# Kernel tuning notes

Measured on AMD Instinct MI355X. Metric: run time of the kernel, lower is better.

The kernel has to match this reference:

```python
import jax, jax.numpy as jnp
import numpy as np

N = 100000   # nodes
E = 1600000  # edges
IN = 128     # input feature dim
HID = 64     # hidden = IN // 2
OUT = 8      # output_size
B = 16384    # lookup batch


def sage_conv(x, src, dst, W_l, W_r, b, n):
    # PyG SAGEConv (aggr='mean', root_weight=True):
    # out = lin_l(mean_{j in N(i)} x_j) + lin_r(x_i)
    msgs = x[src]                                              # [E, F] gather
    agg = jax.ops.segment_sum(msgs, dst, num_segments=n)       # [N, F] scatter-add
    deg = jax.ops.segment_sum(jnp.ones((src.shape[0],), x.dtype), dst, num_segments=n)
    mean = agg / jnp.maximum(deg, 1.0)[:, None]                # zero-degree -> 0
    return mean @ W_l + x @ W_r + b


def setup_inputs() -> dict:
    key = jax.random.key(0)
    ks = jax.random.split(key, 10)
    node_feats = jax.random.normal(ks[0], (N, IN), dtype=jnp.float32)
    edge_index = jax.random.randint(ks[1], (2, E), 0, N, dtype=jnp.int64)
    idx = jax.random.randint(ks[2], (B,), 0, N, dtype=jnp.int64)
    dropout_mask = jax.random.uniform(ks[3], (N, HID), dtype=jnp.float32)
    s1 = 1.0 / np.sqrt(IN)
    s2 = 1.0 / np.sqrt(HID)
    W1_l = jax.random.normal(ks[4], (IN, HID), dtype=jnp.float32) * s1
    W1_r = jax.random.normal(ks[5], (IN, HID), dtype=jnp.float32) * s1
    b1 = jnp.zeros((HID,), dtype=jnp.float32)
    W2_l = jax.random.normal(ks[6], (HID, OUT), dtype=jnp.float32) * s2
    W2_r = jax.random.normal(ks[7], (HID, OUT), dtype=jnp.float32) * s2
    b2 = jnp.zeros((OUT,), dtype=jnp.float32)
    return {"node_feats": node_feats, "edge_index": edge_index, "idx": idx,
            "dropout_mask": dropout_mask, "W1_l": W1_l, "W1_r": W1_r, "b1": b1,
            "W2_l": W2_l, "W2_r": W2_r, "b2": b2}


def reference(node_feats, edge_index, idx, dropout_mask, W1_l, W1_r, b1, W2_l, W2_r, b2):
    n = node_feats.shape[0]
    src, dst = edge_index[0], edge_index[1]
    h = sage_conv(node_feats, src, dst, W1_l, W1_r, b1, n)     # [N, HID]
    h = jax.nn.relu(h)
    keep = (dropout_mask > 0.5).astype(h.dtype)                # F.dropout p=0.5
    h = h * keep * 2.0                                         # inverted dropout scale 1/(1-p)
    emb = sage_conv(h, src, dst, W2_l, W2_r, b2, n)            # [N, OUT]
    return emb[idx]                                            # [B, OUT]
```

## Files before the change

### kernel.cpp

```cpp
#include <hip/hip_runtime.h>
#include <hip/hip_fp16.h>

#define IN_F 128
#define HID_F 64
#define OUT_F 8

#define BSHIFT 7
#define BGRAN 128
#define BCAP 2688
#define NBUK_MAX 784
#define CHUNK 4096
#define EPT (CHUNK / 256)
#define CEPT ((BCAP + 255) / 256)

typedef _Float16 f16x8 __attribute__((ext_vector_type(8)));
typedef float f32x4 __attribute__((ext_vector_type(4)));

__global__ __launch_bounds__(1024) void init_bcur(int* __restrict__ bcur, int nbuk) {
  int t = threadIdx.x;
  if (t < nbuk) bcur[t] = t * BCAP;
}

__global__ __launch_bounds__(256) void bucket_scatter(
    const int* __restrict__ src, const int* __restrict__ dst,
    int* __restrict__ bcur, int* __restrict__ ebuf, int n_edges) {
  __shared__ int hist[NBUK_MAX];
  __shared__ int base[NBUK_MAX];
  int t = threadIdx.x;
  for (int i = t; i < NBUK_MAX; i += 256) hist[i] = 0;
  __syncthreads();
  int e0 = blockIdx.x * CHUNK;
  int pk[EPT];
  int bk[EPT];
#pragma unroll
  for (int k = 0; k < EPT; ++k) {
    int e = e0 + k * 256 + t;
    if (e < n_edges) {
      int s = src[e];
      int d = dst[e];
      bk[k] = d >> BSHIFT;
      pk[k] = ((d & (BGRAN - 1)) << 24) | s;
      atomicAdd(&hist[bk[k]], 1);
    } else {
      bk[k] = -1;
    }
  }
  __syncthreads();
  for (int i = t; i < NBUK_MAX; i += 256) {
    int c = hist[i];
    base[i] = c ? atomicAdd(&bcur[i], c) : 0;
  }
  __syncthreads();
  for (int i = t; i < NBUK_MAX; i += 256) hist[i] = 0;
  __syncthreads();
#pragma unroll
  for (int k = 0; k < EPT; ++k) {
    if (bk[k] >= 0) {
      int r = atomicAdd(&hist[bk[k]], 1);
      ebuf[base[bk[k]] + r] = pk[k];
    }
  }
}

__global__ __launch_bounds__(256) void bucket_csr(
    const int* __restrict__ ebuf, const int* __restrict__ bcur,
    int* __restrict__ offs_f, int* __restrict__ deg_i,
    int* __restrict__ csr_src, int n_nodes) {
  __shared__ int hist[BGRAN];
  __shared__ int cur[BGRAN];
  __shared__ int s[BGRAN];
  __shared__ int lds_src[BCAP];
  int b = blockIdx.x;
  int t = threadIdx.x;
  if (t < BGRAN) hist[t] = 0;
  __syncthreads();
  int beg = b * BCAP;
  int cnt = bcur[b] - beg;
  int pk[CEPT];
  int np = 0;
  for (int j = t; j < cnt; j += 256) {
    pk[np] = ebuf[beg + j];
    atomicAdd(&hist[(unsigned)pk[np] >> 24], 1);
    ++np;
  }
  __syncthreads();
  if (t < BGRAN) s[t] = hist[t];
  __syncthreads();
  for (int d = 1; d < BGRAN; d <<= 1) {
    int v = 0;
    if (t >= d && t < BGRAN) v = s[t - d];
    __syncthreads();
    if (t >= d && t < BGRAN) s[t] += v;
    __syncthreads();
  }
  if (t < BGRAN) {
    int excl = (t == 0) ? 0 : s[t - 1];
    cur[t] = excl;
    int node = b * BGRAN + t;
    if (node < n_nodes) {
      offs_f[node] = beg + excl;
      deg_i[node] = hist[t];
    }
  }
  __syncthreads();
  for (int i = 0; i < np; ++i) {
    int dl = (unsigned)pk[i] >> 24;
    int p = atomicAdd(&cur[dl], 1);
    lds_src[p] = pk[i] & 0xFFFFFF;
  }
  __syncthreads();
  for (int j = t; j < cnt; j += 256) csr_src[beg + j] = lds_src[j];
}

__global__ __launch_bounds__(128) void w_prep(
    const float* __restrict__ Wl, const float* __restrict__ Wr,
    _Float16* __restrict__ Wt) {
  int n = threadIdx.x;
  for (int k = 0; k < IN_F; ++k) {
    float v = (n < HID_F) ? Wl[k * HID_F + n] : Wr[k * HID_F + (n - HID_F)];
    Wt[n * IN_F + k] = (_Float16)v;
  }
}

#define K1_ROWS 128
#define XSH 136
__global__ __launch_bounds__(256) void k1_proj(
    const float* __restrict__ x,
    const _Float16* __restrict__ Wt,
    const float* __restrict__ b1,
    const float* __restrict__ mask,
    __half* __restrict__ y1h,
    __half* __restrict__ r1h,
    unsigned long long* __restrict__ mbits,
    int n_nodes) {
  __shared__ _Float16 XS[K1_ROWS * XSH];
  int tid = threadIdx.x;
  int w = tid >> 6;
  int lane = tid & 63;
  int n0 = blockIdx.x * K1_ROWS;
  int m = lane & 15;
  int quad = lane >> 4;

  for (int i = w * 32; i < w * 32 + 32; ++i) {
    int node = n0 + i;
    if (node < n_nodes) {
      float mv = mask[(size_t)node * HID_F + lane];
      unsigned long long bits = __ballot(mv > 0.5f);
      if (lane == 0) mbits[node] = bits;
    }
  }

  f16x8 af[2][4];
#pragma unroll
  for (int ti = 0; ti < 2; ++ti) {
    int t = w + ti * 4;
#pragma unroll
    for (int kk = 0; kk < 4; ++kk)
      af[ti][kk] = *(const f16x8*)(Wt + (size_t)(t * 16 + m) * IN_F + kk * 32 + quad * 8);
  }
  float4 b1v = *(const float4*)(b1 + w * 16 + quad * 4);

#pragma unroll
  for (int p = 0; p < 16; ++p) {
    int i = tid + p * 256;
    int row = i >> 5;
    int k4 = (i & 31) * 4;
    int gs = min(n0 + row, n_nodes - 1);
    float4 v = *(const float4*)(x + (size_t)gs * IN_F + k4);
    _Float16 hv[4] = {(_Float16)v.x, (_Float16)v.y, (_Float16)v.z, (_Float16)v.w};
    *(uint2*)&XS[row * XSH + k4] = *(uint2*)hv;
  }
  __syncthreads();

#pragma unroll
  for (int rt = 0; rt < 8; ++rt) {
    f32x4 acc0 = f32x4{0.f, 0.f, 0.f, 0.f};
    f32x4 acc1 = f32x4{0.f, 0.f, 0.f, 0.f};
#pragma unroll
    for (int kk = 0; kk < 4; ++kk) {
      f16x8 bx = *(const f16x8*)&XS[(rt * 16 + m) * XSH + kk * 32 + quad * 8];
      acc0 = __builtin_amdgcn_mfma_f32_16x16x32_f16(af[0][kk], bx, acc0, 0, 0, 0);
      acc1 = __builtin_amdgcn_mfma_f32_16x16x32_f16(af[1][kk], bx, acc1, 0, 0, 0);
    }
    int node = n0 + rt * 16 + m;
    if (node < n_nodes) {
      __half hy[4], hr[4];
#pragma unroll
      for (int r = 0; r < 4; ++r) {
        hy[r] = __float2half(acc0[r]);
        hr[r] = __float2half(acc1[r] + ((const float*)&b1v)[r]);
      }
      *(uint2*)(y1h + (size_t)node * HID_F + w * 16 + quad * 4) = *(uint2*)hy;
      *(uint2*)(r1h + (size_t)node * HID_F + w * 16 + quad * 4) = *(uint2*)hr;
    }
  }
}

__global__ __launch_bounds__(256) void agg1_fused(
    const __half* __restrict__ y1h,
    const __half* __restrict__ r1h,
    const int* __restrict__ deg_i,
    const int* __restrict__ offs,
    const int* __restrict__ csr_src,
    const unsigned long long* __restrict__ mbits,
    __half* __restrict__ h_h,
    int n_nodes) {
  int node = (blockIdx.x * blockDim.x + threadIdx.x) >> 6;
  int lane = threadIdx.x & 63;
  if (node >= n_nodes) return;
  int q = lane >> 4;
  int f4 = lane & 15;
  int beg = offs[node];
  int d = deg_i[node];
  const int* cp = csr_src + beg;
  float a0 = 0.f, a1 = 0.f, a2 = 0.f, a3 = 0.f;
  int j = 0;
  for (; j + 16 <= d; j += 16) {
    int s0 = cp[j + q];
    int s1 = cp[j + 4 + q];
    int s2 = cp[j + 8 + q];
    int s3 = cp[j + 12 + q];
    uint2 g0 = *(const uint2*)(y1h + (size_t)s0 * HID_F + f4 * 4);
    uint2 g1 = *(const uint2*)(y1h + (size_t)s1 * HID_F + f4 * 4);
    uint2 g2 = *(const uint2*)(y1h + (size_t)s2 * HID_F + f4 * 4);
    uint2 g3 = *(const uint2*)(y1h + (size_t)s3 * HID_F + f4 * 4);
    float2 p0 = __half22float2(*(const __half2*)&g0.x);
    float2 p1 = __half22float2(*(const __half2*)&g0.y);
    float2 p2 = __half22float2(*(const __half2*)&g1.x);
    float2 p3 = __half22float2(*(const __half2*)&g1.y);
    float2 p4 = __half22float2(*(const __half2*)&g2.x);
    float2 p5 = __half22float2(*(const __half2*)&g2.y);
    float2 p6 = __half22float2(*(const __half2*)&g3.x);
    float2 p7 = __half22float2(*(const __half2*)&g3.y);
    a0 += (p0.x + p2.x) + (p4.x + p6.x);
    a1 += (p0.y + p2.y) + (p4.y + p6.y);
    a2 += (p1.x + p3.x) + (p5.x + p7.x);
    a3 += (p1.y + p3.y) + (p5.y + p7.y);
  }
  for (; j < d; j += 4) {
    int e = j + q;
    if (e < d) {
      int s = cp[e];
      uint2 g = *(const uint2*)(y1h + (size_t)s * HID_F + f4 * 4);
      float2 p0 = __half22float2(*(const __half2*)&g.x);
      float2 p1 = __half22float2(*(const __half2*)&g.y);
      a0 += p0.x; a1 += p0.y; a2 += p1.x; a3 += p1.y;
    }
  }
  a0 += __shfl_xor(a0, 16); a0 += __shfl_xor(a0, 32);
  a1 += __shfl_xor(a1, 16); a1 += __shfl_xor(a1, 32);
  a2 += __shfl_xor(a2, 16); a2 += __shfl_xor(a2, 32);
  a3 += __shfl_xor(a3, 16); a3 += __shfl_xor(a3, 32);
  if (q == 0) {
    float inv = 1.0f / fmaxf((float)d, 1.0f);
    size_t o = (size_t)node * HID_F + f4 * 4;
    uint2 rg = *(const uint2*)(r1h + o);
    float2 r01 = __half22float2(*(const __half2*)&rg.x);
    float2 r23 = __half22float2(*(const __half2*)&rg.y);
    unsigned long long mb = mbits[node];
    float vx = fmaxf(a0 * inv + r01.x, 0.f);
    float vy = fmaxf(a1 * inv + r01.y, 0.f);
    float vz = fmaxf(a2 * inv + r23.x, 0.f);
    float vw = fmaxf(a3 * inv + r23.y, 0.f);
    int fb = f4 * 4;
    vx = ((mb >> (fb + 0)) & 1ull) ? vx * 2.f : 0.f;
    vy = ((mb >> (fb + 1)) & 1ull) ? vy * 2.f : 0.f;
    vz = ((mb >> (fb + 2)) & 1ull) ? vz * 2.f : 0.f;
    vw = ((mb >> (fb + 3)) & 1ull) ? vw * 2.f : 0.f;
    __half hh[4] = {__float2half(vx), __float2half(vy),
                    __float2half(vz), __float2half(vw)};
    *(uint2*)(h_h + o) = *(uint2*)hh;
  }
}

__global__ __launch_bounds__(256) void k3b_z(
    const __half* __restrict__ h_h,
    const float* __restrict__ W2l,
    __half* __restrict__ z,
    int n_nodes) {
  __shared__ float WS[HID_F][OUT_F];
  int tid = threadIdx.x;
  if (tid < 128) {
    float4 w = *(const float4*)(W2l + tid * 4);
    *(float4*)&WS[tid >> 1][(tid & 1) * 4] = w;
  }
  __syncthreads();
  int node = blockIdx.x * blockDim.x + tid;
  if (node >= n_nodes) return;
  const __half* hr = h_h + (size_t)node * HID_F;
  float acc[8] = {0, 0, 0, 0, 0, 0, 0, 0};
  for (int k = 0; k < HID_F; k += 8) {
    uint4 hv = *(const uint4*)(hr + k);
    float2 f0 = __half22float2(*(const __half2*)&hv.x);
    float2 f1 = __half22float2(*(const __half2*)&hv.y);
    float2 f2 = __half22float2(*(const __half2*)&hv.z);
    float2 f3 = __half22float2(*(const __half2*)&hv.w);
    float hh[8] = {f0.x, f0.y, f1.x, f1.y, f2.x, f2.y, f3.x, f3.y};
#pragma unroll
    for (int j = 0; j < 8; ++j) {
      float4 w0 = *(const float4*)&WS[k + j][0];
      float4 w1 = *(const float4*)&WS[k + j][4];
      acc[0] += hh[j] * w0.x; acc[1] += hh[j] * w0.y;
      acc[2] += hh[j] * w0.z; acc[3] += hh[j] * w0.w;
      acc[4] += hh[j] * w1.x; acc[5] += hh[j] * w1.y;
      acc[6] += hh[j] * w1.z; acc[7] += hh[j] * w1.w;
    }
  }
  __half hz[8];
#pragma unroll
  for (int j = 0; j < 8; ++j) hz[j] = __float2half(acc[j]);
  *(uint4*)(z + (size_t)node * OUT_F) = *(uint4*)hz;
}

__global__ __launch_bounds__(256) void out_fused(
    const int* __restrict__ idx,
    const __half* __restrict__ z,
    const int* __restrict__ deg_i,
    const int* __restrict__ offs,
    const int* __restrict__ csr_src,
    const __half* __restrict__ h_h,
    const float* __restrict__ W2r,
    const float* __restrict__ b2,
    float* __restrict__ out,
    int n_batch) {
  int b = (blockIdx.x * blockDim.x + threadIdx.x) >> 6;
  int lane = threadIdx.x & 63;
  if (b >= n_batch) return;
  int i = idx[b];
  int e8 = lane >> 3;
  int o = lane & 7;
  int beg = offs[i];
  int d = deg_i[i];
  float acc = 0.f;
  for (int j = e8; j < d; j += 8) {
    int s = csr_src[beg + j];
    acc += __half2float(z[(size_t)s * OUT_F + o]);
  }
  float dv = fmaxf((float)d, 1.0f);
  float v = acc / dv;
  uint4 hv = *(const uint4*)(h_h + (size_t)i * HID_F + e8 * 8);
  float2 f0 = __half22float2(*(const __half2*)&hv.x);
  float2 f1 = __half22float2(*(const __half2*)&hv.y);
  float2 f2 = __half22float2(*(const __half2*)&hv.z);
  float2 f3 = __half22float2(*(const __half2*)&hv.w);
  float hh[8] = {f0.x, f0.y, f1.x, f1.y, f2.x, f2.y, f3.x, f3.y};
#pragma unroll
  for (int jj = 0; jj < 8; ++jj) {
    int k = e8 * 8 + jj;
    v += hh[jj] * W2r[k * OUT_F + o];
  }
  v += __shfl_xor(v, 8);
  v += __shfl_xor(v, 16);
  v += __shfl_xor(v, 32);
  if (e8 == 0) out[(size_t)b * OUT_F + o] = v + b2[o];
}

extern "C" void kernel_launch(void* const* d_in, const int* in_sizes, int n_in,
                              void* d_out, int out_size, void* d_ws, size_t ws_size,
                              hipStream_t stream) {
  const float* x    = (const float*)d_in[0];
  const int*   ei   = (const int*)d_in[1];
  const int*   idx  = (const int*)d_in[2];
  const float* mask = (const float*)d_in[3];
  const float* W1l  = (const float*)d_in[4];
  const float* W1r  = (const float*)d_in[5];
  const float* b1   = (const float*)d_in[6];
  const float* W2l  = (const float*)d_in[7];
  const float* W2r  = (const float*)d_in[8];
  const float* b2   = (const float*)d_in[9];
  float* out = (float*)d_out;

  int n_nodes = in_sizes[0] / IN_F;
  int n_edges = in_sizes[1] / 2;
  int n_batch = in_sizes[2];
  const int* src = ei;
  const int* dst = ei + n_edges;

  int nbuk = (n_nodes + BGRAN - 1) / BGRAN;
  int nchunk = (n_edges + CHUNK - 1) / CHUNK;

  char* ws = (char*)d_ws;
  size_t off = 0;
  __half* y1h = (__half*)(ws + off); off += (size_t)n_nodes * HID_F * 2;
  __half* r1h = (__half*)(ws + off); off += (size_t)n_nodes * HID_F * 2;
  __half* h_h = (__half*)(ws + off); off += (size_t)n_nodes * HID_F * 2;
  __half* z   = (__half*)(ws + off); off += (size_t)n_nodes * OUT_F * 2;
  unsigned long long* mbits = (unsigned long long*)(ws + off); off += (size_t)n_nodes * 8;
  _Float16* Wt = (_Float16*)(ws + off); off += (size_t)IN_F * IN_F * 2;
  int* ebuf    = (int*)(ws + off); off += (size_t)nbuk * BCAP * 4;
  int* csr_src = (int*)(ws + off); off += (size_t)nbuk * BCAP * 4;
  int* deg_i   = (int*)(ws + off); off += (size_t)n_nodes * 4;
  int* offs_f  = (int*)(ws + off); off += (size_t)n_nodes * 4;
  int* bcur    = (int*)(ws + off); off += NBUK_MAX * 4;

  init_bcur<<<1, 1024, 0, stream>>>(bcur, nbuk);
  w_prep<<<1, 128, 0, stream>>>(W1l, W1r, Wt);
  bucket_scatter<<<nchunk, 256, 0, stream>>>(src, dst, bcur, ebuf, n_edges);
  k1_proj<<<(n_nodes + K1_ROWS - 1) / K1_ROWS, 256, 0, stream>>>(
      x, Wt, b1, mask, y1h, r1h, mbits, n_nodes);
  bucket_csr<<<nbuk, 256, 0, stream>>>(ebuf, bcur, offs_f, deg_i, csr_src, n_nodes);

  {
    long long th = (long long)n_nodes * HID_F;
    agg1_fused<<<(int)((th + 255) / 256), 256, 0, stream>>>(
        y1h, r1h, deg_i, offs_f, csr_src, mbits, h_h, n_nodes);
  }

  k3b_z<<<(n_nodes + 255) / 256, 256, 0, stream>>>(h_h, W2l, z, n_nodes);
  {
    long long th = (long long)n_batch * 64;
    out_fused<<<(int)((th + 255) / 256), 256, 0, stream>>>(
        idx, z, deg_i, offs_f, csr_src, h_h, W2r, b2, out, n_batch);
  }
}
```

Baseline: 256.7 us.

## Pack CSR offset/degree, unroll gathers, batch mask loads, and use wave-shuffle scan

Packs each node's CSR offset and degree into one uint2, so consumers issue a single load instead of two. The bucket prefix scan now uses wave shuffles instead of a barrier-heavy LDS scan. k1_proj batches its mask loads eight at a time to raise memory-level parallelism. agg1_fused unrolls the neighbour gather to 32 edges, handles the tail with clamped indices, and hoists the residual and mask loads ahead of the loop using readfirstlane. out_fused gets the same wave-uniform indexing and a two-way unrolled gather. These are several independent latency-hiding tweaks; they add register pressure in exchange.

```diff
diff --git a/kernel.cpp b/kernel.cpp
--- a/kernel.cpp
+++ b/kernel.cpp
@@ -64,11 +64,10 @@
 
 __global__ __launch_bounds__(256) void bucket_csr(
     const int* __restrict__ ebuf, const int* __restrict__ bcur,
-    int* __restrict__ offs_f, int* __restrict__ deg_i,
-    int* __restrict__ csr_src, int n_nodes) {
+    uint2* __restrict__ nd, int* __restrict__ csr_src, int n_nodes) {
   __shared__ int hist[BGRAN];
   __shared__ int cur[BGRAN];
-  __shared__ int s[BGRAN];
+  __shared__ int excl_s[BGRAN];
   __shared__ int lds_src[BCAP];
   int b = blockIdx.x;
   int t = threadIdx.x;
@@ -84,23 +83,24 @@
     ++np;
   }
   __syncthreads();
-  if (t < BGRAN) s[t] = hist[t];
-  __syncthreads();
-  for (int d = 1; d < BGRAN; d <<= 1) {
-    int v = 0;
-    if (t >= d && t < BGRAN) v = s[t - d];
-    __syncthreads();
-    if (t >= d && t < BGRAN) s[t] += v;
-    __syncthreads();
-  }
+  if (t < 64) {
+    int h0 = hist[2 * t];
+    int h1 = hist[2 * t + 1];
+    int ps = h0 + h1;
+#pragma unroll
+    for (int dd = 1; dd < 64; dd <<= 1) {
+      int u = __shfl_up(ps, dd);
+      if (t >= dd) ps += u;
+    }
+    excl_s[2 * t] = ps - h1 - h0;
+    excl_s[2 * t + 1] = ps - h1;
+  }
+  __syncthreads();
   if (t < BGRAN) {
-    int excl = (t == 0) ? 0 : s[t - 1];
+    int excl = excl_s[t];
     cur[t] = excl;
     int node = b * BGRAN + t;
-    if (node < n_nodes) {
-      offs_f[node] = beg + excl;
-      deg_i[node] = hist[t];
-    }
+    if (node < n_nodes) nd[node] = make_uint2((unsigned)(beg + excl), (unsigned)hist[t]);
   }
   __syncthreads();
   for (int i = 0; i < np; ++i) {
@@ -141,12 +141,19 @@
   int m = lane & 15;
   int quad = lane >> 4;
 
-  for (int i = w * 32; i < w * 32 + 32; ++i) {
-    int node = n0 + i;
-    if (node < n_nodes) {
-      float mv = mask[(size_t)node * HID_F + lane];
-      unsigned long long bits = __ballot(mv > 0.5f);
-      if (lane == 0) mbits[node] = bits;
+#pragma unroll
+  for (int i0 = 0; i0 < 32; i0 += 8) {
+    float mv[8];
+#pragma unroll
+    for (int u = 0; u < 8; ++u) {
+      int node = n0 + w * 32 + i0 + u;
+      mv[u] = (node < n_nodes) ? mask[(size_t)node * HID_F + lane] : 0.f;
+    }
+#pragma unroll
+    for (int u = 0; u < 8; ++u) {
+      int node = n0 + w * 32 + i0 + u;
+      unsigned long long bits = __ballot(mv[u] > 0.5f);
+      if (lane == 0 && node < n_nodes) mbits[node] = bits;
     }
   }
 
@@ -199,8 +206,7 @@
 __global__ __launch_bounds__(256) void agg1_fused(
     const __half* __restrict__ y1h,
     const __half* __restrict__ r1h,
-    const int* __restrict__ deg_i,
-    const int* __restrict__ offs,
+    const uint2* __restrict__ nd,
     const int* __restrict__ csr_src,
     const unsigned long long* __restrict__ mbits,
     __half* __restrict__ h_h,
@@ -208,14 +214,49 @@
   int node = (blockIdx.x * blockDim.x + threadIdx.x) >> 6;
   int lane = threadIdx.x & 63;
   if (node >= n_nodes) return;
+  int nu = __builtin_amdgcn_readfirstlane(node);
   int q = lane >> 4;
   int f4 = lane & 15;
-  int beg = offs[node];
-  int d = deg_i[node];
+
+  uint2 be = nd[nu];
+  unsigned long long mb = mbits[nu];
+  size_t o = (size_t)nu * HID_F + f4 * 4;
+  uint2 rg = *(const uint2*)(r1h + o);
+
+  int beg = (int)be.x;
+  int d = (int)be.y;
   const int* cp = csr_src + beg;
   float a0 = 0.f, a1 = 0.f, a2 = 0.f, a3 = 0.f;
+
+#define ACC4(g)                                              \
+  {                                                          \
+    float2 p0 = __half22float2(*(const __half2*)&(g).x);     \
+    float2 p1 = __half22float2(*(const __half2*)&(g).y);     \
+    a0 += p0.x; a1 += p0.y; a2 += p1.x; a3 += p1.y;          \
+  }
+
   int j = 0;
-  for (; j + 16 <= d; j += 16) {
+  for (; j + 32 <= d; j += 32) {
+    int s0 = cp[j + q];
+    int s1 = cp[j + 4 + q];
+    int s2 = cp[j + 8 + q];
+    int s3 = cp[j + 12 + q];
+    int s4 = cp[j + 16 + q];
+    int s5 = cp[j + 20 + q];
+    int s6 = cp[j + 24 + q];
+    int s7 = cp[j + 28 + q];
+    uint2 g0 = *(const uint2*)(y1h + (size_t)s0 * HID_F + f4 * 4);
+    uint2 g1 = *(const uint2*)(y1h + (size_t)s1 * HID_F + f4 * 4);
+    uint2 g2 = *(const uint2*)(y1h + (size_t)s2 * HID_F + f4 * 4);
+    uint2 g3 = *(const uint2*)(y1h + (size_t)s3 * HID_F + f4 * 4);
+    uint2 g4 = *(const uint2*)(y1h + (size_t)s4 * HID_F + f4 * 4);
+    uint2 g5 = *(const uint2*)(y1h + (size_t)s5 * HID_F + f4 * 4);
+    uint2 g6 = *(const uint2*)(y1h + (size_t)s6 * HID_F + f4 * 4);
+    uint2 g7 = *(const uint2*)(y1h + (size_t)s7 * HID_F + f4 * 4);
+    ACC4(g0) ACC4(g1) ACC4(g2) ACC4(g3)
+    ACC4(g4) ACC4(g5) ACC4(g6) ACC4(g7)
+  }
+  if (j + 16 <= d) {
     int s0 = cp[j + q];
     int s1 = cp[j + 4 + q];
     int s2 = cp[j + 8 + q];
@@ -224,40 +265,35 @@
     uint2 g1 = *(const uint2*)(y1h + (size_t)s1 * HID_F + f4 * 4);
     uint2 g2 = *(const uint2*)(y1h + (size_t)s2 * HID_F + f4 * 4);
     uint2 g3 = *(const uint2*)(y1h + (size_t)s3 * HID_F + f4 * 4);
-    float2 p0 = __half22float2(*(const __half2*)&g0.x);
-    float2 p1 = __half22float2(*(const __half2*)&g0.y);
-    float2 p2 = __half22float2(*(const __half2*)&g1.x);
-    float2 p3 = __half22float2(*(const __half2*)&g1.y);
-    float2 p4 = __half22float2(*(const __half2*)&g2.x);
-    float2 p5 = __half22float2(*(const __half2*)&g2.y);
-    float2 p6 = __half22float2(*(const __half2*)&g3.x);
-    float2 p7 = __half22float2(*(const __half2*)&g3.y);
-    a0 += (p0.x + p2.x) + (p4.x + p6.x);
-    a1 += (p0.y + p2.y) + (p4.y + p6.y);
-    a2 += (p1.x + p3.x) + (p5.x + p7.x);
-    a3 += (p1.y + p3.y) + (p5.y + p7.y);
-  }
-  for (; j < d; j += 4) {
-    int e = j + q;
-    if (e < d) {
-      int s = cp[e];
-      uint2 g = *(const uint2*)(y1h + (size_t)s * HID_F + f4 * 4);
-      float2 p0 = __half22float2(*(const __half2*)&g.x);
-      float2 p1 = __half22float2(*(const __half2*)&g.y);
-      a0 += p0.x; a1 += p0.y; a2 += p1.x; a3 += p1.y;
-    }
-  }
+    ACC4(g0) ACC4(g1) ACC4(g2) ACC4(g3)
+    j += 16;
+  }
+  if (j < d) {
+    int dm = d - 1;
+    int e0 = j + q, e1 = j + 4 + q, e2 = j + 8 + q, e3 = j + 12 + q;
+    int s0 = cp[min(e0, dm)];
+    int s1 = cp[min(e1, dm)];
+    int s2 = cp[min(e2, dm)];
+    int s3 = cp[min(e3, dm)];
+    uint2 g0 = *(const uint2*)(y1h + (size_t)s0 * HID_F + f4 * 4);
+    uint2 g1 = *(const uint2*)(y1h + (size_t)s1 * HID_F + f4 * 4);
+    uint2 g2 = *(const uint2*)(y1h + (size_t)s2 * HID_F + f4 * 4);
+    uint2 g3 = *(const uint2*)(y1h + (size_t)s3 * HID_F + f4 * 4);
+    if (e0 < d) ACC4(g0)
+    if (e1 < d) ACC4(g1)
+    if (e2 < d) ACC4(g2)
+    if (e3 < d) ACC4(g3)
+  }
+#undef ACC4
+
   a0 += __shfl_xor(a0, 16); a0 += __shfl_xor(a0, 32);
   a1 += __shfl_xor(a1, 16); a1 += __shfl_xor(a1, 32);
   a2 += __shfl_xor(a2, 16); a2 += __shfl_xor(a2, 32);
   a3 += __shfl_xor(a3, 16); a3 += __shfl_xor(a3, 32);
   if (q == 0) {
     float inv = 1.0f / fmaxf((float)d, 1.0f);
-    size_t o = (size_t)node * HID_F + f4 * 4;
-    uint2 rg = *(const uint2*)(r1h + o);
     float2 r01 = __half22float2(*(const __half2*)&rg.x);
     float2 r23 = __half22float2(*(const __half2*)&rg.y);
-    unsigned long long mb = mbits[node];
     float vx = fmaxf(a0 * inv + r01.x, 0.f);
     float vy = fmaxf(a1 * inv + r01.y, 0.f);
     float vz = fmaxf(a2 * inv + r23.x, 0.f);
@@ -315,8 +351,7 @@
 __global__ __launch_bounds__(256) void out_fused(
     const int* __restrict__ idx,
     const __half* __restrict__ z,
-    const int* __restrict__ deg_i,
-    const int* __restrict__ offs,
+    const uint2* __restrict__ nd,
     const int* __restrict__ csr_src,
     const __half* __restrict__ h_h,
     const float* __restrict__ W2r,
@@ -326,19 +361,28 @@
   int b = (blockIdx.x * blockDim.x + threadIdx.x) >> 6;
   int lane = threadIdx.x & 63;
   if (b >= n_batch) return;
-  int i = idx[b];
+  int bu = __builtin_amdgcn_readfirstlane(b);
+  int i = idx[bu];
+  int iu = __builtin_amdgcn_readfirstlane(i);
   int e8 = lane >> 3;
   int o = lane & 7;
-  int beg = offs[i];
-  int d = deg_i[i];
+  uint2 be = nd[iu];
+  uint4 hv = *(const uint4*)(h_h + (size_t)iu * HID_F + e8 * 8);
+  int beg = (int)be.x;
+  int d = (int)be.y;
+  const int* cp = csr_src + beg;
   float acc = 0.f;
-  for (int j = e8; j < d; j += 8) {
-    int s = csr_src[beg + j];
-    acc += __half2float(z[(size_t)s * OUT_F + o]);
-  }
+  int j = e8;
+  for (; j + 8 < d; j += 16) {
+    int s0 = cp[j];
+    int s1 = cp[j + 8];
+    float z0 = __half2float(z[(size_t)s0 * OUT_F + o]);
+    float z1 = __half2float(z[(size_t)s1 * OUT_F + o]);
+    acc += z0 + z1;
+  }
+  if (j < d) acc += __half2float(z[(size_t)cp[j] * OUT_F + o]);
   float dv = fmaxf((float)d, 1.0f);
   float v = acc / dv;
-  uint4 hv = *(const uint4*)(h_h + (size_t)i * HID_F + e8 * 8);
   float2 f0 = __half22float2(*(const __half2*)&hv.x);
   float2 f1 = __half22float2(*(const __half2*)&hv.y);
   float2 f2 = __half22float2(*(const __half2*)&hv.z);
@@ -389,8 +433,7 @@
   _Float16* Wt = (_Float16*)(ws + off); off += (size_t)IN_F * IN_F * 2;
   int* ebuf    = (int*)(ws + off); off += (size_t)nbuk * BCAP * 4;
   int* csr_src = (int*)(ws + off); off += (size_t)nbuk * BCAP * 4;
-  int* deg_i   = (int*)(ws + off); off += (size_t)n_nodes * 4;
-  int* offs_f  = (int*)(ws + off); off += (size_t)n_nodes * 4;
+  uint2* nd    = (uint2*)(ws + off); off += (size_t)n_nodes * 8;
   int* bcur    = (int*)(ws + off); off += NBUK_MAX * 4;
 
   init_bcur<<<1, 1024, 0, stream>>>(bcur, nbuk);
@@ -398,18 +441,18 @@
   bucket_scatter<<<nchunk, 256, 0, stream>>>(src, dst, bcur, ebuf, n_edges);
   k1_proj<<<(n_nodes + K1_ROWS - 1) / K1_ROWS, 256, 0, stream>>>(
       x, Wt, b1, mask, y1h, r1h, mbits, n_nodes);
-  bucket_csr<<<nbuk, 256, 0, stream>>>(ebuf, bcur, offs_f, deg_i, csr_src, n_nodes);
+  bucket_csr<<<nbuk, 256, 0, stream>>>(ebuf, bcur, nd, csr_src, n_nodes);
 
   {
     long long th = (long long)n_nodes * HID_F;
     agg1_fused<<<(int)((th + 255) / 256), 256, 0, stream>>>(
-        y1h, r1h, deg_i, offs_f, csr_src, mbits, h_h, n_nodes);
+        y1h, r1h, nd, csr_src, mbits, h_h, n_nodes);
   }
 
   k3b_z<<<(n_nodes + 255) / 256, 256, 0, stream>>>(h_h, W2l, z, n_nodes);
   {
     long long th = (long long)n_batch * 64;
     out_fused<<<(int)((th + 255) / 256), 256, 0, stream>>>(
-        idx, z, deg_i, offs_f, csr_src, h_h, W2r, b2, out, n_batch);
-  }
-}
+        idx, z, nd, csr_src, h_h, W2r, b2, out, n_batch);
+  }
+}
```

After: 246.0 us. -4.2%, faster.
